# Kernel tuning notes

Hardware: AMD Instinct MI355X
Metric: run time of the kernel (lower is better)

The kernel has to match this reference:

```python
import jax, jax.numpy as jnp
import numpy as np

N_LEVELS = 2 ** 4 - 1  # 4-bit uniform quantization -> 15 intervals


def fake_quant(x, lower, upper):
    """Uniform asymmetric fake-quantization with straight-through rounding.
    clamp to [lower, upper], quantize to 4-bit grid, dequantize."""
    scale = (upper - lower) / N_LEVELS
    xc = jnp.clip(x, lower, upper)
    q = (xc - lower) / scale
    # straight-through estimator for round
    q = q + jax.lax.stop_gradient(jnp.round(q) - q)
    return q * scale + lower


def setup_inputs() -> dict:
    key = jax.random.key(0)
    kA, kB = jax.random.split(key)
    A = jax.random.normal(kA, (128, 8, 256, 64), dtype=jnp.float32)
    B = jax.random.normal(kB, (128, 8, 64, 256), dtype=jnp.float32)
    # learnable per-tensor bounds (as found by init_quantization_scale search)
    a_lower = jnp.full((1,), -2.5, dtype=jnp.float32)
    a_upper = jnp.full((1,), 2.5, dtype=jnp.float32)
    b_lower = jnp.full((1,), -2.5, dtype=jnp.float32)
    b_upper = jnp.full((1,), 2.5, dtype=jnp.float32)
    return {"A": A, "B": B, "a_lower": a_lower, "a_upper": a_upper,
            "b_lower": b_lower, "b_upper": b_upper}


def reference(A, B, a_lower, a_upper, b_lower, b_upper):
    Aq = fake_quant(A, a_lower, a_upper)
    Bq = fake_quant(B, b_lower, b_upper)
    # batched matmul: [bw, h, n, d] @ [bw, h, d, n] -> [bw, h, n, n]
    return jnp.einsum('bhnd,bhdm->bhnm', Aq, Bq)
```

## Files before the change

### kernel.cpp

```cpp
#include <hip/hip_runtime.h>

typedef __attribute__((ext_vector_type(4))) int   int4v;
typedef __attribute__((ext_vector_type(4))) float float4v;

__device__ __forceinline__ int swz(int row, int slot) {
    return slot ^ ((row ^ (row >> 2)) & 3);
}

__device__ __forceinline__ int quant1(float x, float lo, float up, float scale) {
    float xc = fminf(fmaxf(x, lo), up);
    return (int)rintf((xc - lo) / scale);
}

__global__ __launch_bounds__(256, 4) void qmm_i8_kernel(
    const float* __restrict__ A, const float* __restrict__ B,
    const float* __restrict__ aLo, const float* __restrict__ aUp,
    const float* __restrict__ bLo, const float* __restrict__ bUp,
    float* __restrict__ Out)
{
    __shared__ int   qA[256 * 16];
    __shared__ int   qB[256 * 16];
    __shared__ float RAf[256];
    __shared__ float CBf[256];

    const int tid = threadIdx.x;
    const int b   = blockIdx.x;

    const float lA = aLo[0], uA = aUp[0];
    const float lB = bLo[0], uB = bUp[0];
    const float sA  = (uA - lA) / 15.0f;
    const float sB  = (uB - lB) / 15.0f;
    const float sAB = sA * sB;

    const float4v* A4 = (const float4v*)(A + (size_t)b * 256 * 64);
    const float4v* B4 = (const float4v*)(B + (size_t)b * 64 * 256);
    float* outb = Out + (size_t)b * 256 * 256;

    #pragma unroll
    for (int it = 0; it < 16; ++it) {
        int f = it * 256 + tid;
        float4v v = A4[f];
        int q0 = quant1(v[0], lA, uA, sA);
        int q1 = quant1(v[1], lA, uA, sA);
        int q2 = quant1(v[2], lA, uA, sA);
        int q3 = quant1(v[3], lA, uA, sA);
        int p  = q0 | (q1 << 8) | (q2 << 16) | (q3 << 24);
        int row = f >> 4, chunk = f & 15;
        qA[row * 16 + swz(row, chunk >> 2) * 4 + (chunk & 3)] = p;
    }

    const int u  = tid & 63;
    const int kg = tid >> 6;
    #pragma unroll
    for (int kb = 0; kb < 4; ++kb) {
        int k0 = kb * 16 + kg * 4;
        int q[4][4];
        #pragma unroll
        for (int r = 0; r < 4; ++r) {
            float4v v = B4[(size_t)(k0 + r) * 64 + u];
            q[r][0] = quant1(v[0], lB, uB, sB);
            q[r][1] = quant1(v[1], lB, uB, sB);
            q[r][2] = quant1(v[2], lB, uB, sB);
            q[r][3] = quant1(v[3], lB, uB, sB);
        }
        #pragma unroll
        for (int c = 0; c < 4; ++c) {
            int col = u * 4 + c;
            int p = q[0][c] | (q[1][c] << 8) | (q[2][c] << 16) | (q[3][c] << 24);
            qB[col * 16 + swz(col, kb) * 4 + kg] = p;
        }
    }

    __syncthreads();

    {
        unsigned sa = 0, sb = 0;
        #pragma unroll
        for (int j = 0; j < 16; ++j) {
            unsigned pa = (unsigned)qA[tid * 16 + swz(tid, j >> 2) * 4 + (j & 3)];
            unsigned pb = (unsigned)qB[tid * 16 + swz(tid, j >> 2) * 4 + (j & 3)];
            sa += (pa * 0x01010101u) >> 24;
            sb += (pb * 0x01010101u) >> 24;
        }
        float c32 = 32.0f * lA * lB;
        RAf[tid] = sA * lB * (float)sa + c32;
        CBf[tid] = lA * sB * (float)sb + c32;
    }
    __syncthreads();

    const int wave = tid >> 6, lane = tid & 63;
    const int lr = lane & 15;
    const int lk = lane >> 4;

    int4v afrag[4];
    #pragma unroll
    for (int rt = 0; rt < 4; ++rt) {
        int row = wave * 64 + rt * 16 + lr;
        afrag[rt] = *(const int4v*)&qA[row * 16 + swz(row, lk) * 4];
    }

    #pragma unroll 4
    for (int ct = 0; ct < 16; ++ct) {
        int col = ct * 16 + lr;
        int4v bfrag = *(const int4v*)&qB[col * 16 + swz(col, lk) * 4];
        float cb = CBf[col];
        #pragma unroll
        for (int rt = 0; rt < 4; ++rt) {
            int4v acc = {0, 0, 0, 0};
            acc = __builtin_amdgcn_mfma_i32_16x16x64_i8(afrag[rt], bfrag, acc, 0, 0, 0);
            int orow = wave * 64 + rt * 16 + lk * 4;
            #pragma unroll
            for (int r = 0; r < 4; ++r) {
                outb[(size_t)(orow + r) * 256 + col] =
                    sAB * (float)acc[r] + RAf[orow + r] + cb;
            }
        }
    }
}

extern "C" void kernel_launch(void* const* d_in, const int* in_sizes, int n_in,
                              void* d_out, int out_size, void* d_ws, size_t ws_size,
                              hipStream_t stream) {
    const float* A   = (const float*)d_in[0];
    const float* B   = (const float*)d_in[1];
    const float* aLo = (const float*)d_in[2];
    const float* aUp = (const float*)d_in[3];
    const float* bLo = (const float*)d_in[4];
    const float* bUp = (const float*)d_in[5];
    float* Out = (float*)d_out;

    int batches = in_sizes[0] / (256 * 64);
    qmm_i8_kernel<<<batches, 256, 0, stream>>>(A, B, aLo, aUp, bLo, bUp, Out);
}
```

Before: 100.6 us.

## Quantize A directly into MFMA fragments and store output as float4 rows

A is no longer staged through shared memory. Each lane loads its own row slice, quantizes it into the MFMA fragment, and computes row sums with wave shuffles. The MFMA operands are swapped so every lane holds four consecutive output columns, which allows float4 nontemporal stores in place of scalar strided stores. B is packed into 128-bit LDS writes, and the loads are marked nontemporal. This cuts LDS traffic and store instructions, at the cost of more complex fragment indexing and changed correctness constants (c64 split).

```diff
diff --git a/kernel.cpp b/kernel.cpp
--- a/kernel.cpp
+++ b/kernel.cpp
@@ -12,15 +12,22 @@
     return (int)rintf((xc - lo) / scale);
 }
 
-__global__ __launch_bounds__(256, 4) void qmm_i8_kernel(
+__device__ __forceinline__ int qpack4(float4v v, float lo, float up, float sc) {
+    return  quant1(v[0], lo, up, sc)        | (quant1(v[1], lo, up, sc) << 8) |
+           (quant1(v[2], lo, up, sc) << 16) | (quant1(v[3], lo, up, sc) << 24);
+}
+
+__device__ __forceinline__ unsigned bsum(int p) {
+    return ((unsigned)p * 0x01010101u) >> 24;
+}
+
+__global__ __launch_bounds__(256, 4) void qmm_kernel(
     const float* __restrict__ A, const float* __restrict__ B,
     const float* __restrict__ aLo, const float* __restrict__ aUp,
     const float* __restrict__ bLo, const float* __restrict__ bUp,
     float* __restrict__ Out)
 {
-    __shared__ int   qA[256 * 16];
     __shared__ int   qB[256 * 16];
-    __shared__ float RAf[256];
     __shared__ float CBf[256];
 
     const int tid = threadIdx.x;
@@ -36,84 +43,81 @@
     const float4v* B4 = (const float4v*)(B + (size_t)b * 64 * 256);
     float* outb = Out + (size_t)b * 256 * 256;
 
-    #pragma unroll
-    for (int it = 0; it < 16; ++it) {
-        int f = it * 256 + tid;
-        float4v v = A4[f];
-        int q0 = quant1(v[0], lA, uA, sA);
-        int q1 = quant1(v[1], lA, uA, sA);
-        int q2 = quant1(v[2], lA, uA, sA);
-        int q3 = quant1(v[3], lA, uA, sA);
-        int p  = q0 | (q1 << 8) | (q2 << 16) | (q3 << 24);
-        int row = f >> 4, chunk = f & 15;
-        qA[row * 16 + swz(row, chunk >> 2) * 4 + (chunk & 3)] = p;
-    }
-
-    const int u  = tid & 63;
-    const int kg = tid >> 6;
-    #pragma unroll
-    for (int kb = 0; kb < 4; ++kb) {
-        int k0 = kb * 16 + kg * 4;
-        int q[4][4];
+    {
+        const int u = tid & 63, w = tid >> 6;
+        int pk[4][4];
         #pragma unroll
-        for (int r = 0; r < 4; ++r) {
-            float4v v = B4[(size_t)(k0 + r) * 64 + u];
-            q[r][0] = quant1(v[0], lB, uB, sB);
-            q[r][1] = quant1(v[1], lB, uB, sB);
-            q[r][2] = quant1(v[2], lB, uB, sB);
-            q[r][3] = quant1(v[3], lB, uB, sB);
+        for (int m = 0; m < 4; ++m) {
+            float4v r0 = __builtin_nontemporal_load(&B4[(size_t)(w*16 + m*4 + 0) * 64 + u]);
+            float4v r1 = __builtin_nontemporal_load(&B4[(size_t)(w*16 + m*4 + 1) * 64 + u]);
+            float4v r2 = __builtin_nontemporal_load(&B4[(size_t)(w*16 + m*4 + 2) * 64 + u]);
+            float4v r3 = __builtin_nontemporal_load(&B4[(size_t)(w*16 + m*4 + 3) * 64 + u]);
+            #pragma unroll
+            for (int c = 0; c < 4; ++c) {
+                pk[c][m] =  quant1(r0[c], lB, uB, sB)        | (quant1(r1[c], lB, uB, sB) << 8) |
+                           (quant1(r2[c], lB, uB, sB) << 16) | (quant1(r3[c], lB, uB, sB) << 24);
+            }
         }
         #pragma unroll
         for (int c = 0; c < 4; ++c) {
             int col = u * 4 + c;
-            int p = q[0][c] | (q[1][c] << 8) | (q[2][c] << 16) | (q[3][c] << 24);
-            qB[col * 16 + swz(col, kb) * 4 + kg] = p;
+            int4v v = {pk[c][0], pk[c][1], pk[c][2], pk[c][3]};
+            *(int4v*)&qB[col * 16 + swz(col, w) * 4] = v;
         }
     }
-
     __syncthreads();
 
     {
-        unsigned sa = 0, sb = 0;
+        unsigned s = 0;
         #pragma unroll
-        for (int j = 0; j < 16; ++j) {
-            unsigned pa = (unsigned)qA[tid * 16 + swz(tid, j >> 2) * 4 + (j & 3)];
-            unsigned pb = (unsigned)qB[tid * 16 + swz(tid, j >> 2) * 4 + (j & 3)];
-            sa += (pa * 0x01010101u) >> 24;
-            sb += (pb * 0x01010101u) >> 24;
+        for (int sl = 0; sl < 4; ++sl) {
+            int4v v = *(const int4v*)&qB[tid * 16 + swz(tid, sl) * 4];
+            s += bsum(v[0]) + bsum(v[1]) + bsum(v[2]) + bsum(v[3]);
         }
-        float c32 = 32.0f * lA * lB;
-        RAf[tid] = sA * lB * (float)sa + c32;
-        CBf[tid] = lA * sB * (float)sb + c32;
+        CBf[tid] = lA * sB * (float)s;
+    }
+
+    const int lane = tid & 63, wave = tid >> 6;
+    const int lr = lane & 15, lk = lane >> 4;
+    const float c64 = 64.0f * lA * lB;
+
+    int4v afrag[4];
+    float RA[4];
+    #pragma unroll
+    for (int rt = 0; rt < 4; ++rt) {
+        int row = wave * 64 + rt * 16 + lr;
+        const float4v* ap = A4 + (size_t)row * 16 + lk * 4;
+        float4v x0 = __builtin_nontemporal_load(ap + 0);
+        float4v x1 = __builtin_nontemporal_load(ap + 1);
+        float4v x2 = __builtin_nontemporal_load(ap + 2);
+        float4v x3 = __builtin_nontemporal_load(ap + 3);
+        int p0 = qpack4(x0, lA, uA, sA), p1 = qpack4(x1, lA, uA, sA);
+        int p2 = qpack4(x2, lA, uA, sA), p3 = qpack4(x3, lA, uA, sA);
+        int4v f = {p0, p1, p2, p3};
+        afrag[rt] = f;
+        int rs = (int)(bsum(p0) + bsum(p1) + bsum(p2) + bsum(p3));
+        rs += __shfl_xor(rs, 16);
+        rs += __shfl_xor(rs, 32);
+        RA[rt] = sA * lB * (float)rs + c64;
     }
     __syncthreads();
 
-    const int wave = tid >> 6, lane = tid & 63;
-    const int lr = lane & 15;
-    const int lk = lane >> 4;
-
-    int4v afrag[4];
-    #pragma unroll
-    for (int rt = 0; rt < 4; ++rt) {
-        int row = wave * 64 + rt * 16 + lr;
-        afrag[rt] = *(const int4v*)&qA[row * 16 + swz(row, lk) * 4];
-    }
-
-    #pragma unroll 4
+    const int4v z4 = {0, 0, 0, 0};
+    #pragma unroll 2
     for (int ct = 0; ct < 16; ++ct) {
         int col = ct * 16 + lr;
-        int4v bfrag = *(const int4v*)&qB[col * 16 + swz(col, lk) * 4];
-        float cb = CBf[col];
+        int4v  bfrag = *(const int4v*)&qB[col * 16 + swz(col, lk) * 4];
+        float4v cb   = *(const float4v*)&CBf[ct * 16 + lk * 4];
         #pragma unroll
         for (int rt = 0; rt < 4; ++rt) {
-            int4v acc = {0, 0, 0, 0};
-            acc = __builtin_amdgcn_mfma_i32_16x16x64_i8(afrag[rt], bfrag, acc, 0, 0, 0);
-            int orow = wave * 64 + rt * 16 + lk * 4;
-            #pragma unroll
-            for (int r = 0; r < 4; ++r) {
-                outb[(size_t)(orow + r) * 256 + col] =
-                    sAB * (float)acc[r] + RAf[orow + r] + cb;
-            }
+            int4v acc = __builtin_amdgcn_mfma_i32_16x16x64_i8(bfrag, afrag[rt], z4, 0, 0, 0);
+            int row = wave * 64 + rt * 16 + lr;
+            float4v o;
+            o[0] = fmaf(sAB, (float)acc[0], RA[rt] + cb[0]);
+            o[1] = fmaf(sAB, (float)acc[1], RA[rt] + cb[1]);
+            o[2] = fmaf(sAB, (float)acc[2], RA[rt] + cb[2]);
+            o[3] = fmaf(sAB, (float)acc[3], RA[rt] + cb[3]);
+            __builtin_nontemporal_store(o, (float4v*)&outb[(size_t)row * 256 + ct * 16 + lk * 4]);
         }
     }
 }
@@ -130,5 +134,5 @@
     float* Out = (float*)d_out;
 
     int batches = in_sizes[0] / (256 * 64);
-    qmm_i8_kernel<<<batches, 256, 0, stream>>>(A, B, aLo, aUp, bLo, bUp, Out);
+    qmm_kernel<<<batches, 256, 0, stream>>>(A, B, aLo, aUp, bLo, bUp, Out);
 }
```

New measurement: 121.2 us. 1.2x slower.
